# Kernel optimization log

Measured on AMD Instinct MI355X. Metric: run time of the kernel, lower is better.

The kernel has to match this reference:

```python
import jax, jax.numpy as jnp
import numpy as np

B, D, K = 65536, 128, 8
BOUND = 3.0
MIN_BIN_W = 1e-3   # min_bin_width
MIN_BIN_H = 1e-3   # min_bin_height
MIN_DERIV = 1e-3   # min_derivative
EPS = 1e-6


def setup_inputs() -> dict:
    key = jax.random.key(0)
    k1, k2, k3, k4 = jax.random.split(key, 4)
    return {
        "x": jax.random.normal(k1, (B, D), jnp.float32) * 1.5,
        "unnormalized_widths": jax.random.normal(k2, (D, K), jnp.float32),
        "unnormalized_heights": jax.random.normal(k3, (D, K), jnp.float32),
        "unnormalized_derivatives": jax.random.normal(k4, (D, K - 1), jnp.float32),
    }


def _calculate_knots(lengths, lower, upper):
    # lengths: [D, K] summing to ~1 -> scaled lengths and knot positions [D, K+1]
    knots = jnp.cumsum(lengths, axis=-1)
    knots = jnp.pad(knots, ((0, 0), (1, 0)))
    knots = (upper - lower) * knots + lower
    knots = knots.at[..., 0].set(lower)
    knots = knots.at[..., -1].set(upper)
    return knots[..., 1:] - knots[..., :-1], knots


def _select_bins(p, idx):
    # p: [D, Kp] per-dim tables, idx: [B, D] bin indices -> [B, D]
    i = jnp.clip(idx, 0, p.shape[-1] - 1)
    return p[jnp.arange(p.shape[0])[None, :], i]


def _spline_forward(x, uw, uh, ud):
    w = jax.nn.softmax(uw, axis=-1)
    h = jax.nn.softmax(uh, axis=-1)
    d = jax.nn.softplus(ud)

    num_bins = w.shape[-1]
    widths = MIN_BIN_W + (1.0 - MIN_BIN_W * num_bins) * w
    heights = MIN_BIN_H + (1.0 - MIN_BIN_H * num_bins) * h
    derivs = jnp.pad(MIN_DERIV + d, ((0, 0), (1, 1)), constant_values=1.0 - MIN_DERIV)  # [D, K+1]

    widths, cumwidths = _calculate_knots(widths, -BOUND, BOUND)
    heights, cumheights = _calculate_knots(heights, -BOUND, BOUND)

    inside = (x >= -BOUND) & (x <= BOUND)
    xc = jnp.clip(x, -BOUND, BOUND)  # keep tail values finite; masked out below

    # searchsorted: which bin each input falls into   [B, D]
    bin_idx = jnp.sum(xc[..., None] >= (cumwidths + EPS)[None, :, :], axis=-1) - 1

    iw = _select_bins(widths, bin_idx)
    icw = _select_bins(cumwidths, bin_idx)
    ich = _select_bins(cumheights, bin_idx)
    idelta = _select_bins(heights / widths, bin_idx)
    id0 = _select_bins(derivs, bin_idx)
    id1 = _select_bins(derivs[..., 1:], bin_idx)
    ih = _select_bins(heights, bin_idx)

    # rational quadratic spline (forward)
    theta = (xc - icw) / iw
    t1m = theta * (1.0 - theta)
    numerator = ih * (idelta * theta ** 2 + id0 * t1m)
    denominator = idelta + (id0 + id1 - 2.0 * idelta) * t1m
    out = ich + numerator / denominator
    dnum = idelta ** 2 * (id1 * theta ** 2 + 2.0 * idelta * t1m + id0 * (1.0 - theta) ** 2)
    lad = jnp.log(dnum) - 2.0 * jnp.log(denominator)

    u = jnp.where(inside, out, x)          # identity outside tail bound
    lad = jnp.where(inside, lad, 0.0)
    return u, lad


def reference(x, unnormalized_widths, unnormalized_heights, unnormalized_derivatives):
    u, lad = _spline_forward(x, unnormalized_widths, unnormalized_heights, unnormalized_derivatives)
    log_detJ = jnp.sum(lad, axis=1)
    return u, log_detJ
```

## Files before the change

kernel.cpp:

```cpp
#include <hip/hip_runtime.h>
#include <math.h>

namespace {
constexpr int D = 128;
constexpr int K = 8;
constexpr float BOUND = 3.0f;
constexpr float EPS = 1e-6f;
constexpr float MIN_BIN_W = 1e-3f;
constexpr float MIN_BIN_H = 1e-3f;
constexpr float MIN_DERIV = 1e-3f;
constexpr float LN2 = 0.6931471805599453f;
constexpr int WPB = 8;
constexpr int RPW = 8;
}

template <int CTRL, int ROWM>
__device__ __forceinline__ float dpp_add(float v) {
    const int t = __builtin_amdgcn_update_dpp(0, __float_as_int(v), CTRL, ROWM, 0xf, true);
    return v + __int_as_float(t);
}

__device__ __forceinline__ float wave_sum_dpp(float v) {
    v = dpp_add<0x111, 0xf>(v);
    v = dpp_add<0x112, 0xf>(v);
    v = dpp_add<0x114, 0xf>(v);
    v = dpp_add<0x118, 0xf>(v);
    v = dpp_add<0x142, 0xa>(v);
    v = dpp_add<0x143, 0xc>(v);
    return v;
}

__device__ __forceinline__ float spline_elem(float xv, int slot, const float* kn,
                                             const float4* __restrict__ A,
                                             const float4* __restrict__ B,
                                             float* __restrict__ outp) {
    const bool inside = (xv >= -BOUND) & (xv <= BOUND);
    const float xc = fminf(fmaxf(xv, -BOUND), BOUND);
    int idx = 0;
    #pragma unroll
    for (int j = 0; j < 7; ++j) idx += (xc >= kn[j]) ? 1 : 0;
    const float4 ra = A[idx * D + slot];
    const float4 rb = B[idx * D + slot];
    const float theta = (xc - ra.x) * ra.y;
    const float omt   = 1.f - theta;
    const float t1m   = theta * omt;
    const float th2   = theta * theta;
    const float num   = rb.y * (ra.w * th2 + ra.z * t1m);
    const float den   = ra.w + rb.w * t1m;
    const float rd    = __builtin_amdgcn_rcpf(den);
    const float outv  = fmaf(num, rd, rb.x);
    const float dnum  = ra.w * ra.w * (rb.z * th2 + 2.f * ra.w * t1m + ra.z * omt * omt);
    const float lad   = __log2f(dnum * rd * rd);
    *outp = inside ? outv : xv;
    return inside ? lad : 0.f;
}

__global__ __launch_bounds__(512, 6) void spline_fwd(
    const float* __restrict__ x,
    const float* __restrict__ uw,
    const float* __restrict__ uh,
    const float* __restrict__ ud,
    float* __restrict__ out_u,
    float* __restrict__ out_ld,
    int nrows)
{
    __shared__ __align__(16) float4 s_A[K * D];
    __shared__ __align__(16) float4 s_B[K * D];

    const int tid = threadIdx.x;
    if (tid < D) {
        const int d = tid;
        float wv[K], hv[K], cw[K + 1], ch[K + 1], der[K + 1];

        {
            const float* p = uw + d * K;
            float m = p[0];
            #pragma unroll
            for (int j = 1; j < K; ++j) m = fmaxf(m, p[j]);
            float s = 0.f;
            #pragma unroll
            for (int j = 0; j < K; ++j) { wv[j] = __expf(p[j] - m); s += wv[j]; }
            const float inv = (1.f - MIN_BIN_W * K) / s;
            #pragma unroll
            for (int j = 0; j < K; ++j) wv[j] = MIN_BIN_W + wv[j] * inv;
        }
        {
            const float* p = uh + d * K;
            float m = p[0];
            #pragma unroll
            for (int j = 1; j < K; ++j) m = fmaxf(m, p[j]);
            float s = 0.f;
            #pragma unroll
            for (int j = 0; j < K; ++j) { hv[j] = __expf(p[j] - m); s += hv[j]; }
            const float inv = (1.f - MIN_BIN_H * K) / s;
            #pragma unroll
            for (int j = 0; j < K; ++j) hv[j] = MIN_BIN_H + hv[j] * inv;
        }
        cw[0] = -BOUND; ch[0] = -BOUND;
        float cs_w = 0.f, cs_h = 0.f;
        #pragma unroll
        for (int j = 0; j < K; ++j) {
            cs_w += wv[j]; cw[j + 1] = 2.f * BOUND * cs_w - BOUND;
            cs_h += hv[j]; ch[j + 1] = 2.f * BOUND * cs_h - BOUND;
        }
        cw[K] = BOUND; ch[K] = BOUND;

        der[0] = 1.f - MIN_DERIV;
        der[K] = 1.f - MIN_DERIV;
        {
            const float* p = ud + d * (K - 1);
            #pragma unroll
            for (int j = 1; j < K; ++j) {
                const float v = p[j - 1];
                const float sp = log1pf(__expf(-fabsf(v))) + fmaxf(v, 0.f);
                der[j] = MIN_DERIV + sp;
            }
        }

        const int slot = (d & 1) * 64 + (d >> 1);
        #pragma unroll
        for (int j = 0; j < K; ++j) {
            const float w  = cw[j + 1] - cw[j];
            const float h  = ch[j + 1] - ch[j];
            const float iw = 1.f / w;
            const float dl = h * iw;
            s_A[j * D + slot] = make_float4(cw[j], iw, der[j], dl);
            s_B[j * D + slot] = make_float4(ch[j], h, der[j + 1],
                                            der[j] + der[j + 1] - 2.f * dl);
        }
    }
    __syncthreads();

    const int wave = tid >> 6;
    const int lane = tid & 63;
    const int slot0 = lane;
    const int slot1 = 64 + lane;

    float kn0[7], kn1[7];
    #pragma unroll
    for (int j = 0; j < 7; ++j) {
        kn0[j] = s_A[(j + 1) * D + slot0].x + EPS;
        kn1[j] = s_A[(j + 1) * D + slot1].x + EPS;
    }

    const int r0 = (blockIdx.x * WPB + wave) * RPW;
    const int lo2 = lane * 2;

    #pragma unroll
    for (int i = 0; i < RPW; ++i) {
        const int r = r0 + i;
        const float2 xv = *(const float2*)(x + (size_t)r * D + lo2);
        float u0, u1;
        float la = spline_elem(xv.x, slot0, kn0, s_A, s_B, &u0)
                 + spline_elem(xv.y, slot1, kn1, s_A, s_B, &u1);
        *(float2*)(out_u + (size_t)r * D + lo2) = make_float2(u0, u1);

        la = wave_sum_dpp(la);
        if (lane == 63) out_ld[r] = la * LN2;
    }
}

extern "C" void kernel_launch(void* const* d_in, const int* in_sizes, int n_in,
                              void* d_out, int out_size, void* d_ws, size_t ws_size,
                              hipStream_t stream) {
    const float* x  = (const float*)d_in[0];
    const float* uw = (const float*)d_in[1];
    const float* uh = (const float*)d_in[2];
    const float* ud = (const float*)d_in[3];
    const int nrows = in_sizes[0] / D;
    float* out_u  = (float*)d_out;
    float* out_ld = (float*)d_out + (size_t)nrows * D;
    const int nblocks = nrows / (WPB * RPW);
    spline_fwd<<<nblocks, 512, 0, stream>>>(x, uw, uh, ud, out_u, out_ld, nrows);
}
```

Measured before the change: 96.91 us.

## Prefetch all row inputs, use packed float2 math, merge per-pair log2

Each wave now issues all eight x-row loads up front before any compute, so global memory latency overlaps instead of being paid once per row. The spline arithmetic for the two elements each lane handles is written on float2 vectors so the compiler can emit packed FP32 instructions. The two per-lane log2 calls become one log2 of the product. Outside-bound handling switches to adding (x - clamped x) to the spline output instead of a select. The two shared tables are merged into one array. Risks: more registers live from the prefetch, and small rounding or overflow differences from the merged log and the additive tail handling.

```diff
diff --git a/kernel.cpp b/kernel.cpp
--- a/kernel.cpp
+++ b/kernel.cpp
@@ -13,6 +13,8 @@
 constexpr int WPB = 8;
 constexpr int RPW = 8;
 }
+
+typedef float v2f __attribute__((ext_vector_type(2)));
 
 template <int CTRL, int ROWM>
 __device__ __forceinline__ float dpp_add(float v) {
@@ -30,31 +32,6 @@
     return v;
 }
 
-__device__ __forceinline__ float spline_elem(float xv, int slot, const float* kn,
-                                             const float4* __restrict__ A,
-                                             const float4* __restrict__ B,
-                                             float* __restrict__ outp) {
-    const bool inside = (xv >= -BOUND) & (xv <= BOUND);
-    const float xc = fminf(fmaxf(xv, -BOUND), BOUND);
-    int idx = 0;
-    #pragma unroll
-    for (int j = 0; j < 7; ++j) idx += (xc >= kn[j]) ? 1 : 0;
-    const float4 ra = A[idx * D + slot];
-    const float4 rb = B[idx * D + slot];
-    const float theta = (xc - ra.x) * ra.y;
-    const float omt   = 1.f - theta;
-    const float t1m   = theta * omt;
-    const float th2   = theta * theta;
-    const float num   = rb.y * (ra.w * th2 + ra.z * t1m);
-    const float den   = ra.w + rb.w * t1m;
-    const float rd    = __builtin_amdgcn_rcpf(den);
-    const float outv  = fmaf(num, rd, rb.x);
-    const float dnum  = ra.w * ra.w * (rb.z * th2 + 2.f * ra.w * t1m + ra.z * omt * omt);
-    const float lad   = __log2f(dnum * rd * rd);
-    *outp = inside ? outv : xv;
-    return inside ? lad : 0.f;
-}
-
 __global__ __launch_bounds__(512, 6) void spline_fwd(
     const float* __restrict__ x,
     const float* __restrict__ uw,
@@ -64,8 +41,7 @@
     float* __restrict__ out_ld,
     int nrows)
 {
-    __shared__ __align__(16) float4 s_A[K * D];
-    __shared__ __align__(16) float4 s_B[K * D];
+    __shared__ __align__(16) float4 s_T[2 * K * D];
 
     const int tid = threadIdx.x;
     if (tid < D) {
@@ -124,9 +100,9 @@
             const float h  = ch[j + 1] - ch[j];
             const float iw = 1.f / w;
             const float dl = h * iw;
-            s_A[j * D + slot] = make_float4(cw[j], iw, der[j], dl);
-            s_B[j * D + slot] = make_float4(ch[j], h, der[j + 1],
-                                            der[j] + der[j + 1] - 2.f * dl);
+            s_T[j * D + slot] = make_float4(cw[j], iw, der[j], dl);
+            s_T[K * D + j * D + slot] = make_float4(ch[j], h, der[j + 1],
+                                                    der[j] + der[j + 1] - 2.f * dl);
         }
     }
     __syncthreads();
@@ -135,28 +111,73 @@
     const int lane = tid & 63;
     const int slot0 = lane;
     const int slot1 = 64 + lane;
+    const float4* __restrict__ pa0 = s_T + slot0;
+    const float4* __restrict__ pa1 = s_T + slot1;
 
     float kn0[7], kn1[7];
     #pragma unroll
     for (int j = 0; j < 7; ++j) {
-        kn0[j] = s_A[(j + 1) * D + slot0].x + EPS;
-        kn1[j] = s_A[(j + 1) * D + slot1].x + EPS;
+        kn0[j] = pa0[(j + 1) * D].x + EPS;
+        kn1[j] = pa1[(j + 1) * D].x + EPS;
     }
 
     const int r0 = (blockIdx.x * WPB + wave) * RPW;
     const int lo2 = lane * 2;
+    const float* __restrict__ xbase = x + (size_t)r0 * D + lo2;
+    float* __restrict__ ubase = out_u + (size_t)r0 * D + lo2;
+
+    float2 xs[RPW];
+    #pragma unroll
+    for (int i = 0; i < RPW; ++i)
+        xs[i] = *(const float2*)(xbase + (size_t)i * D);
 
     #pragma unroll
     for (int i = 0; i < RPW; ++i) {
-        const int r = r0 + i;
-        const float2 xv = *(const float2*)(x + (size_t)r * D + lo2);
-        float u0, u1;
-        float la = spline_elem(xv.x, slot0, kn0, s_A, s_B, &u0)
-                 + spline_elem(xv.y, slot1, kn1, s_A, s_B, &u1);
-        *(float2*)(out_u + (size_t)r * D + lo2) = make_float2(u0, u1);
+        const float xv0 = xs[i].x, xv1 = xs[i].y;
+        const float xc0 = fminf(fmaxf(xv0, -BOUND), BOUND);
+        const float xc1 = fminf(fmaxf(xv1, -BOUND), BOUND);
+        const bool in0 = fabsf(xv0) <= BOUND;
+        const bool in1 = fabsf(xv1) <= BOUND;
+
+        int i0 = 0, i1 = 0;
+        #pragma unroll
+        for (int j = 0; j < 7; ++j) {
+            i0 += (xc0 >= kn0[j]) ? 1 : 0;
+            i1 += (xc1 >= kn1[j]) ? 1 : 0;
+        }
+
+        const float4 ra0 = pa0[i0 * D];
+        const float4 rb0 = pa0[i0 * D + K * D];
+        const float4 ra1 = pa1[i1 * D];
+        const float4 rb1 = pa1[i1 * D + K * D];
+
+        const v2f xc  = {xc0, xc1};
+        const v2f xw  = {xv0, xv1};
+        const v2f icw = {ra0.x, ra1.x}, inw = {ra0.y, ra1.y};
+        const v2f d0  = {ra0.z, ra1.z}, dl  = {ra0.w, ra1.w};
+        const v2f ich = {rb0.x, rb1.x}, ih  = {rb0.y, rb1.y};
+        const v2f d1  = {rb0.z, rb1.z}, E   = {rb0.w, rb1.w};
+
+        const v2f theta = (xc - icw) * inw;
+        const v2f omt   = (v2f)1.f - theta;
+        const v2f t1m   = theta * omt;
+        const v2f th2   = theta * theta;
+        const v2f num   = ih * (dl * th2 + d0 * t1m);
+        const v2f den   = dl + E * t1m;
+        const v2f rd    = {__builtin_amdgcn_rcpf(den.x), __builtin_amdgcn_rcpf(den.y)};
+        const v2f outv  = num * rd + ich;
+        const v2f dnum  = (dl * dl) * (d1 * th2 + (dl + dl) * t1m + d0 * (omt * omt));
+        const v2f P     = dnum * (rd * rd);
+
+        const v2f u = outv + (xw - xc);
+        *(float2*)(ubase + (size_t)i * D) = make_float2(u.x, u.y);
+
+        const float P0 = in0 ? P.x : 1.f;
+        const float P1 = in1 ? P.y : 1.f;
+        float la = __log2f(P0 * P1);
 
         la = wave_sum_dpp(la);
-        if (lane == 63) out_ld[r] = la * LN2;
+        if (lane == 63) out_ld[r0 + i] = la * LN2;
     }
 }
 
```

After: 96.29 us. No clear change (-0.6%).
